# Kernel tuning notes

Hardware: AMD Instinct MI355X
Metric: run time of the kernel (lower is better)

Reference implementation:

```python
import jax, jax.numpy as jnp
import numpy as np

N_NODES, N_EDGES, N_ROOTS = 32768, 131072, 1024
VOCAB, EMB_D, FEAT = 50000, 256, 128
SEQ, HEADS, OUT_CH = 16, 16, 125
KERNELS = (5, 6, 7, 8)


def _add_self_loops(edge_index, n):
    loop = jnp.arange(n, dtype=edge_index.dtype)
    src = jnp.concatenate([edge_index[0], loop])
    dst = jnp.concatenate([edge_index[1], loop])
    return src, dst


def _gat_conv(x, W, a_src, a_dst, b, src, dst, n):
    # PyG GATConv (heads=1): h=xW, e_ij = LeakyReLU(a_s.h_j + a_d.h_i), softmax over incoming edges of i
    h = x @ W                                   # [N, F]
    al_s = h @ a_src                            # [N]
    al_d = h @ a_dst                            # [N]
    e = jax.nn.leaky_relu(al_s[src] + al_d[dst], 0.2)   # [E+N]
    m = jax.ops.segment_max(e, dst, num_segments=n)
    ex = jnp.exp(e - m[dst])
    den = jax.ops.segment_sum(ex, dst, num_segments=n)
    coef = ex / den[dst]
    out = jax.ops.segment_sum(coef[:, None] * h[src], dst, num_segments=n)
    return out + b


def _gcn_conv(x, W, b, src, dst, n):
    h = x @ W
    ones = jnp.ones_like(src, dtype=x.dtype)
    deg = jax.ops.segment_sum(ones, dst, num_segments=n)
    dinv = jax.lax.rsqrt(jnp.maximum(deg, 1.0))
    norm = dinv[src] * dinv[dst]                # [E+N]
    out = jax.ops.segment_sum(norm[:, None] * h[src], dst, num_segments=n)
    return out + b


def _transformer_block(x, Wq, bq, Wk, bk, Wv, bv, Wo, bo, g, be):
    # multi-head self-attention + output proj + residual + layernorm (attn_dropout=0)
    n, s, d = x.shape
    dh = d // HEADS
    q = (x @ Wq + bq).reshape(n, s, HEADS, dh)
    k = (x @ Wk + bk).reshape(n, s, HEADS, dh)
    v = (x @ Wv + bv).reshape(n, s, HEADS, dh)
    att = jnp.einsum('nqhd,nkhd->nhqk', q, k) / np.sqrt(dh).astype(np.float32)
    att = jax.nn.softmax(att, axis=-1)
    o = jnp.einsum('nhqk,nkhd->nqhd', att, v).reshape(n, s, d)
    o = o @ Wo + bo
    y = x + o
    mu = jnp.mean(y, axis=-1, keepdims=True)
    var = jnp.var(y, axis=-1, keepdims=True)
    return (y - mu) * jax.lax.rsqrt(var + 1e-5) * g + be


def _conv_branch(t, ws, bs):
    # t: [N, D, S]; Conv1d VALID + ReLU + max-pool over full output length
    feats = []
    for w, b in zip(ws, bs):
        a = jax.lax.conv_general_dilated(t, w, (1,), 'VALID',
                                         dimension_numbers=('NCH', 'OIH', 'NCH'))
        a = jax.nn.relu(a + b[:, None])
        feats.append(jnp.max(a, axis=-1))       # [N, OUT_CH]
    return jnp.concatenate(feats, axis=1)        # [N, 4*OUT_CH]


def _forward(x2, emb, Wq, bq, Wk, bk, Wv, bv, Wo, bo, ln_g, ln_b,
             gat1_W, gat1_as, gat1_ad, gat1_b, gcn1_W, gcn1_b,
             gat2_W, gat2_as, gat2_ad, gat2_b, gcn2_W, gcn2_b,
             conv_w0, conv_b0, conv_w1, conv_b1, conv_w2, conv_b2, conv_w3, conv_b3,
             fc1_W, fc1_b, fc2_W, fc2_b,
             text2, edge_index, root_index, rootpost_index):
    n = x2.shape[0]
    src, dst = _add_self_loops(edge_index, n)

    stance_graph = _gat_conv(x2, gat1_W, gat1_as, gat1_ad, gat1_b, src, dst, n)
    stance_shared = _gcn_conv(x2, gcn1_W, gcn1_b, src, dst, n)

    t = emb[text2]                                            # [N, S, D]
    t = _transformer_block(t, Wq, bq, Wk, bk, Wv, bv, Wo, bo, ln_g, ln_b)
    t_avg = jnp.mean(t, axis=1)                               # [N, D]

    cat = jnp.concatenate([stance_graph, stance_shared, t_avg], axis=1)  # [N, 2F+D]
    stance_graph2 = _gat_conv(cat, gat2_W, gat2_as, gat2_ad, gat2_b, src, dst, n)
    _ = _gcn_conv(stance_shared, gcn2_W, gcn2_b, src, dst, n)  # computed but unused in forward (faithful)

    tc = jnp.transpose(t, (0, 2, 1))                          # [N, D, S]
    text_feat = _conv_branch(tc, (conv_w0, conv_w1, conv_w2, conv_w3),
                             (conv_b0, conv_b1, conv_b2, conv_b3))  # [N, 500]

    final = jnp.concatenate([stance_graph2[root_index],
                             text_feat[root_index],
                             text_feat[rootpost_index]], axis=1)     # [B, F+1000]
    h = jax.nn.relu(final @ fc1_W + fc1_b)
    return h @ fc2_W + fc2_b                                  # [B, 3]


def setup_inputs() -> dict:
    key = jax.random.key(0)
    ks = iter(jax.random.split(key, 48))
    s = 0.05
    inp = {}
    inp['x2'] = jax.random.normal(next(ks), (N_NODES, FEAT), jnp.float32)
    inp['emb'] = jax.random.normal(next(ks), (VOCAB, EMB_D), jnp.float32) * s
    for nm in ['Wq', 'Wk', 'Wv', 'Wo']:
        inp[nm] = jax.random.normal(next(ks), (EMB_D, EMB_D), jnp.float32) * s
    for nm in ['bq', 'bk', 'bv', 'bo']:
        inp[nm] = jnp.zeros((EMB_D,), jnp.float32)
    inp['ln_g'] = jnp.ones((EMB_D,), jnp.float32)
    inp['ln_b'] = jnp.zeros((EMB_D,), jnp.float32)
    inp['gat1_W'] = jax.random.normal(next(ks), (FEAT, FEAT), jnp.float32) * s
    inp['gat1_as'] = jax.random.normal(next(ks), (FEAT,), jnp.float32) * s
    inp['gat1_ad'] = jax.random.normal(next(ks), (FEAT,), jnp.float32) * s
    inp['gat1_b'] = jnp.zeros((FEAT,), jnp.float32)
    inp['gcn1_W'] = jax.random.normal(next(ks), (FEAT, FEAT), jnp.float32) * s
    inp['gcn1_b'] = jnp.zeros((FEAT,), jnp.float32)
    inp['gat2_W'] = jax.random.normal(next(ks), (2 * FEAT + EMB_D, FEAT), jnp.float32) * s
    inp['gat2_as'] = jax.random.normal(next(ks), (FEAT,), jnp.float32) * s
    inp['gat2_ad'] = jax.random.normal(next(ks), (FEAT,), jnp.float32) * s
    inp['gat2_b'] = jnp.zeros((FEAT,), jnp.float32)
    inp['gcn2_W'] = jax.random.normal(next(ks), (FEAT, FEAT), jnp.float32) * s
    inp['gcn2_b'] = jnp.zeros((FEAT,), jnp.float32)
    for i, K in enumerate(KERNELS):
        inp[f'conv_w{i}'] = jax.random.normal(next(ks), (OUT_CH, EMB_D, K), jnp.float32) * s
        inp[f'conv_b{i}'] = jnp.zeros((OUT_CH,), jnp.float32)
    inp['fc1_W'] = jax.random.normal(next(ks), (FEAT + 8 * OUT_CH, 300), jnp.float32) * s
    inp['fc1_b'] = jnp.zeros((300,), jnp.float32)
    inp['fc2_W'] = jax.random.normal(next(ks), (300, 3), jnp.float32) * s
    inp['fc2_b'] = jnp.zeros((3,), jnp.float32)
    inp['text2'] = jax.random.randint(next(ks), (N_NODES, SEQ), 0, VOCAB, jnp.int32)
    inp['edge_index'] = jax.random.randint(next(ks), (2, N_EDGES), 0, N_NODES, jnp.int32)
    inp['root_index'] = jax.random.randint(next(ks), (N_ROOTS,), 0, N_NODES, jnp.int32)
    inp['rootpost_index'] = jax.random.randint(next(ks), (N_ROOTS,), 0, N_NODES, jnp.int32)
    return inp


def reference(x2, emb, Wq, bq, Wk, bk, Wv, bv, Wo, bo, ln_g, ln_b,
              gat1_W, gat1_as, gat1_ad, gat1_b, gcn1_W, gcn1_b,
              gat2_W, gat2_as, gat2_ad, gat2_b, gcn2_W, gcn2_b,
              conv_w0, conv_b0, conv_w1, conv_b1, conv_w2, conv_b2, conv_w3, conv_b3,
              fc1_W, fc1_b, fc2_W, fc2_b,
              text2, edge_index, root_index, rootpost_index):
    return _forward(x2, emb, Wq, bq, Wk, bk, Wv, bv, Wo, bo, ln_g, ln_b,
                    gat1_W, gat1_as, gat1_ad, gat1_b, gcn1_W, gcn1_b,
                    gat2_W, gat2_as, gat2_ad, gat2_b, gcn2_W, gcn2_b,
                    conv_w0, conv_b0, conv_w1, conv_b1, conv_w2, conv_b2, conv_w3, conv_b3,
                    fc1_W, fc1_b, fc2_W, fc2_b,
                    text2, edge_index, root_index, rootpost_index)
```

## Files before the change

### kernel.cpp

```cpp
#include <hip/hip_runtime.h>
#include <hip/hip_bf16.h>
#include <cstdint>
#include <cstddef>

#define N_NODES 32768
#define N_EDGES 131072
#define ET_EDGES (N_EDGES + N_NODES)
#define N_ROOTS 1024
#define EMB_D 256
#define FEAT 128
#define SEQ 16
#define OUT_CH 125

static inline int cdiv(long long a, long long b) { return (int)((a + b - 1) / b); }

typedef short short8 __attribute__((ext_vector_type(8)));
typedef short short4v __attribute__((ext_vector_type(4)));
typedef float f32x4 __attribute__((ext_vector_type(4)));

__device__ __forceinline__ float warpReduceSum(float v) {
#pragma unroll
    for (int m = 32; m; m >>= 1) v += __shfl_xor(v, m, 64);
    return v;
}
__device__ __forceinline__ int encf(float f) {
    int i = __float_as_int(f);
    return i >= 0 ? i : (i ^ 0x7fffffff);
}
__device__ __forceinline__ float decf(int i) {
    return __int_as_float(i >= 0 ? i : (i ^ 0x7fffffff));
}
__device__ __forceinline__ short f2bs(float x) {
    unsigned u = __float_as_uint(x);
    u += 0x7fffu + ((u >> 16) & 1u);
    return (short)(u >> 16);
}
__device__ __forceinline__ short2 f2bs2(float a, float b) {
    union {
        __hip_bfloat162 h;
        short2 s;
    } u;
    u.h = __float22bfloat162_rn(make_float2(a, b));
    return u.s;
}
__device__ __forceinline__ float bs2f(short s) {
    return __uint_as_float(((unsigned)(unsigned short)s) << 16);
}

__global__ void fill_i32(int* p, int v, int n) {
    int i = blockIdx.x * 256 + threadIdx.x;
    if (i < n) p[i] = v;
}

__global__ void init_cat(float* __restrict__ cat, const float* __restrict__ b1, const float* __restrict__ b2) {
    int i = blockIdx.x * 256 + threadIdx.x;
    int n = i >> 8, c = i & 255;
    float b = (c < 128) ? b1[c] : b2[c - 128];
    cat[(size_t)n * 512 + c] = b;
}

__global__ void repack_wall(const float* __restrict__ cw0, const float* __restrict__ cw1,
                            const float* __restrict__ cw2, const float* __restrict__ cw3,
                            __hip_bfloat16* __restrict__ wall) {
    int i = blockIdx.x * 256 + threadIdx.x;
    if (i >= 512 * 2048) return;
    int r = i >> 11, c = i & 2047;
    int k = c >> 8, ic = c & 255;
    float v = 0.f;
    if (r < 500) {
        int Kidx = r / 125, oc = r - Kidx * 125;
        int K = 5 + Kidx;
        if (k < K) {
            const float* cw = Kidx == 0 ? cw0 : Kidx == 1 ? cw1 : Kidx == 2 ? cw2 : cw3;
            v = cw[((size_t)oc * 256 + ic) * K + k];
        }
    }
    wall[i] = __float2bfloat16(v);
}

__global__ void repack_xf(const float* __restrict__ Wq, const float* __restrict__ Wk, const float* __restrict__ Wv,
                          const float* __restrict__ Wo, const float* __restrict__ bq, const float* __restrict__ bk,
                          const float* __restrict__ bv, short* __restrict__ wqkvT, short* __restrict__ woT,
                          float* __restrict__ bqkv) {
    int i = blockIdx.x * 256 + threadIdx.x;
    if (i < 768 * 256) {
        int n = i >> 8, k = i & 255;
        const float* W = n < 256 ? Wq : n < 512 ? Wk : Wv;
        wqkvT[i] = f2bs(W[k * 256 + (n & 255)]);
    }
    if (i < 256 * 256) {
        int n = i >> 8, k = i & 255;
        woT[i] = f2bs(Wo[k * 256 + n]);
    }
    if (i < 768) bqkv[i] = i < 256 ? bq[i] : i < 512 ? bk[i - 256] : bv[i - 512];
}

__global__ void repack_wT(const float* __restrict__ W, short* __restrict__ out, int K, int N) {
    int i = blockIdx.x * 256 + threadIdx.x;
    if (i >= K * N) return;
    int n = i / K, k = i - n * K;
    out[i] = f2bs(W[(size_t)k * N + n]);
}

__global__ __launch_bounds__(256) void mfma_gemm_n128(const float* __restrict__ A, const short* __restrict__ Wt,
                                                      float* __restrict__ C, int K) {
    __shared__ short As[128 * 40];
    __shared__ short Bs[128 * 40];
    const int m0 = blockIdx.x * 128;
    const int tid = threadIdx.x;
    const int lane = tid & 63;
    const int wave = tid >> 6;
    const int wm = (wave >> 1) * 64, wn = (wave & 1) * 64;
    const int quad = lane >> 4, l16 = lane & 15;

    const int r0 = tid >> 2, kc = (tid & 3) * 8;
    const int r1 = r0 + 64;

    f32x4 acc[4][4];
#pragma unroll
    for (int i = 0; i < 4; i++)
#pragma unroll
        for (int j = 0; j < 4; j++) acc[i][j] = (f32x4){0.f, 0.f, 0.f, 0.f};

    for (int k0 = 0; k0 < K; k0 += 32) {
#pragma unroll
        for (int rr = 0; rr < 2; rr++) {
            const int r = rr ? r1 : r0;
            const float* pa = A + (size_t)(m0 + r) * K + k0 + kc;
            float4 a0 = ((const float4*)pa)[0], a1 = ((const float4*)pa)[1];
            short2 c0 = f2bs2(a0.x, a0.y), c1 = f2bs2(a0.z, a0.w), c2 = f2bs2(a1.x, a1.y), c3 = f2bs2(a1.z, a1.w);
            *(short8*)(As + r * 40 + kc) = (short8){c0.x, c0.y, c1.x, c1.y, c2.x, c2.y, c3.x, c3.y};
        }
        *(short8*)(Bs + r0 * 40 + kc) = *(const short8*)(Wt + (size_t)r0 * K + k0 + kc);
        *(short8*)(Bs + r1 * 40 + kc) = *(const short8*)(Wt + (size_t)r1 * K + k0 + kc);
        __syncthreads();
        short8 af[4], bfr[4];
#pragma unroll
        for (int i = 0; i < 4; i++) af[i] = *(const short8*)(As + (wm + i * 16 + l16) * 40 + quad * 8);
#pragma unroll
        for (int j = 0; j < 4; j++) bfr[j] = *(const short8*)(Bs + (wn + j * 16 + l16) * 40 + quad * 8);
#pragma unroll
        for (int i = 0; i < 4; i++)
#pragma unroll
            for (int j = 0; j < 4; j++)
                acc[i][j] = __builtin_amdgcn_mfma_f32_16x16x32_bf16(af[i], bfr[j], acc[i][j], 0, 0, 0);
        __syncthreads();
    }
#pragma unroll
    for (int i = 0; i < 4; i++) {
#pragma unroll
        for (int j = 0; j < 4; j++) {
            const int col = wn + j * 16 + l16;
            const size_t base = (size_t)(m0 + wm + i * 16 + quad * 4) * 128 + col;
#pragma unroll
            for (int r = 0; r < 4; r++) C[base + (size_t)r * 128] = acc[i][j][r];
        }
    }
}

__global__ __launch_bounds__(256) void gemm64(const float* __restrict__ A, const float* __restrict__ B,
                                              const float* __restrict__ bias, float* __restrict__ C,
                                              int M, int N, int K, int lda, int ldc, int doRelu) {
    __shared__ float As[16][65];
    __shared__ float Bs[16][65];
    const int bm = blockIdx.y * 64, bn = blockIdx.x * 64;
    const int tid = threadIdx.x;
    const int tx = tid & 15, ty = tid >> 4;
    float acc[4][4] = {};
    for (int k0 = 0; k0 < K; k0 += 16) {
#pragma unroll
        for (int j = 0; j < 4; j++) {
            int i = tid + j * 256;
            int kk = i & 15, m = i >> 4;
            int gr = bm + m, gc = k0 + kk;
            As[kk][m] = (gr < M && gc < K) ? A[(size_t)gr * lda + gc] : 0.f;
        }
#pragma unroll
        for (int j = 0; j < 4; j++) {
            int i = tid + j * 256;
            int n = i & 63, kk = i >> 6;
            int gr = k0 + kk, gc = bn + n;
            Bs[kk][n] = (gr < K && gc < N) ? B[(size_t)gr * N + gc] : 0.f;
        }
        __syncthreads();
#pragma unroll
        for (int kk = 0; kk < 16; kk++) {
            float a[4], b[4];
#pragma unroll
            for (int i2 = 0; i2 < 4; i2++) a[i2] = As[kk][ty * 4 + i2];
#pragma unroll
            for (int j2 = 0; j2 < 4; j2++) b[j2] = Bs[kk][tx * 4 + j2];
#pragma unroll
            for (int i2 = 0; i2 < 4; i2++)
#pragma unroll
                for (int j2 = 0; j2 < 4; j2++) acc[i2][j2] = fmaf(a[i2], b[j2], acc[i2][j2]);
        }
        __syncthreads();
    }
#pragma unroll
    for (int i2 = 0; i2 < 4; i2++) {
        int r = bm + ty * 4 + i2;
        if (r >= M) continue;
#pragma unroll
        for (int j2 = 0; j2 < 4; j2++) {
            int c = bn + tx * 4 + j2;
            if (c >= N) continue;
            float v = acc[i2][j2];
            if (bias) v += bias[c];
            if (doRelu) v = fmaxf(v, 0.f);
            C[(size_t)r * ldc + c] = v;
        }
    }
}

__global__ __launch_bounds__(256) void alpha_kernel(const float* __restrict__ h, const float* __restrict__ asrc,
                                                    const float* __restrict__ adst, float* __restrict__ als,
                                                    float* __restrict__ ald) {
    int gw = (blockIdx.x * 256 + threadIdx.x) >> 6;
    int lane = threadIdx.x & 63;
    if (gw >= N_NODES) return;
    const float* row = h + (size_t)gw * FEAT;
    float v0 = row[lane], v1 = row[lane + 64];
    float ps = v0 * asrc[lane] + v1 * asrc[lane + 64];
    float pd = v0 * adst[lane] + v1 * adst[lane + 64];
    ps = warpReduceSum(ps);
    pd = warpReduceSum(pd);
    if (lane == 0) {
        als[gw] = ps;
        ald[gw] = pd;
    }
}

__device__ __forceinline__ void edge_decode(int i, const int* __restrict__ ei, int& s, int& d) {
    if (i < N_EDGES) {
        s = ei[i];
        d = ei[N_EDGES + i];
    } else {
        s = d = i - N_EDGES;
    }
}

__global__ void edge_p1(const int* __restrict__ ei, const float* __restrict__ als, const float* __restrict__ ald,
                        float* __restrict__ elog, int* __restrict__ menc, float* dega) {
    int i = blockIdx.x * 256 + threadIdx.x;
    if (i >= ET_EDGES) return;
    int s, d;
    edge_decode(i, ei, s, d);
    float e = als[s] + ald[d];
    e = (e >= 0.f) ? e : 0.2f * e;
    elog[i] = e;
    atomicMax(&menc[d], encf(e));
    if (dega) unsafeAtomicAdd(&dega[d], 1.f);
}

__global__ void edge_p2(const int* __restrict__ ei, float* __restrict__ elog, const int* __restrict__ menc,
                        float* __restrict__ den) {
    int i = blockIdx.x * 256 + threadIdx.x;
    if (i >= ET_EDGES) return;
    int s, d;
    edge_decode(i, ei, s, d);
    float ex = __expf(elog[i] - decf(menc[d]));
    elog[i] = ex;
    unsafeAtomicAdd(&den[d], ex);
}

__global__ void edge_p2b(const int* __restrict__ ei, float* __restrict__ elog, const float* __restrict__ den) {
    int i = blockIdx.x * 256 + threadIdx.x;
    if (i >= ET_EDGES) return;
    int s, d;
    edge_decode(i, ei, s, d);
    elog[i] = elog[i] / den[d];
}

__global__ void dinv_kernel(float* deg) {
    int i = blockIdx.x * 256 + threadIdx.x;
    if (i < N_NODES) deg[i] = rsqrtf(fmaxf(deg[i], 1.f));
}

__global__ void edge_scatter(const int* __restrict__ ei, const float* __restrict__ coef, const float* __restrict__ h,
                             float* __restrict__ out, int ldo) {
    int i = blockIdx.x * 256 + threadIdx.x;
    if (i >= ET_EDGES * FEAT) return;
    int e = i >> 7, f = i & 127;
    int s, d;
    edge_decode(e, ei, s, d);
    unsafeAtomicAdd(&out[(size_t)d * ldo + f], coef[e] * h[(size_t)s * FEAT + f]);
}

__global__ void gcn_scatter(const int* __restrict__ ei, const float* __restrict__ dinv, const float* __restrict__ h,
                            float* __restrict__ out, int ldo) {
    int i = blockIdx.x * 256 + threadIdx.x;
    if (i >= ET_EDGES * FEAT) return;
    int e = i >> 7, f = i & 127;
    int s, d;
    edge_decode(e, ei, s, d);
    float coef = dinv[s] * dinv[d];
    unsafeAtomicAdd(&out[(size_t)d * ldo + f], coef * h[(size_t)s * FEAT + f]);
}

__global__ void root_gather(const float* __restrict__ g2, const int* __restrict__ rooti, const float* __restrict__ gb,
                            float* __restrict__ fin) {
    int i = blockIdx.x * 256 + threadIdx.x;
    if (i >= N_ROOTS * FEAT) return;
    int r = i >> 7, c = i & 127;
    fin[(size_t)r * 1128 + c] = g2[(size_t)rooti[r] * FEAT + c] + gb[c];
}

__global__ void fc2_kernel(const float* __restrict__ fch, const float* __restrict__ W, const float* __restrict__ b,
                           float* __restrict__ out) {
    int i = blockIdx.x * 256 + threadIdx.x;
    if (i >= N_ROOTS * 3) return;
    int r = i / 3, c = i - r * 3;
    float acc = b[c];
    for (int k = 0; k < 300; k++) acc = fmaf(fch[(size_t)r * 300 + k], W[k * 3 + c], acc);
    out[i] = acc;
}

__device__ __forceinline__ int lsw(int row, int col) {
    return row * 256 + (col ^ ((row & 7) << 3));
}

__device__ __forceinline__ int vt_addr(int d, int key) {
    return d * 32 + (((key & 24) ^ (((d ^ (d >> 2)) & 3) << 3)) | (key & 7));
}

template <int MODE>
__global__ __launch_bounds__(256, 3) void xformer_kernel(
    const float* __restrict__ emb, const int* __restrict__ text2, const short* __restrict__ wqkvT,
    const float* __restrict__ bqkv, const short* __restrict__ woT, const float* __restrict__ bo,
    const float* __restrict__ lng, const float* __restrict__ lnb, const int* __restrict__ rooti,
    const int* __restrict__ rpi, float* __restrict__ cat, unsigned short* __restrict__ tbuf) {
    __shared__ short qa[32 * 256];
    __shared__ short kreg[32 * 256];
    __shared__ short vbuf[32 * 256];

    const int tid = threadIdx.x;
    const int wave = tid >> 6, lane = tid & 63;
    const int quad = lane >> 4, l16 = lane & 15;

    int gnode[2];
#pragma unroll
    for (int m = 0; m < 2; m++) {
        int slot = blockIdx.x * 2 + m;
        gnode[m] = (MODE == 0) ? slot : ((slot < N_ROOTS) ? rooti[slot] : rpi[slot - N_ROOTS]);
    }

    {
        const int row = tid >> 3, seg = tid & 7;
        const int m = row >> 4, r = row & 15;
        const int tok = text2[gnode[m] * SEQ + r];
        const float* ep = emb + (size_t)tok * 256 + seg * 32;
#pragma unroll
        for (int j = 0; j < 4; j++) {
            float4 ea = ((const float4*)(ep + j * 8))[0];
            float4 eb = ((const float4*)(ep + j * 8))[1];
            short2 w0 = f2bs2(ea.x, ea.y), w1 = f2bs2(ea.z, ea.w);
            short2 w2 = f2bs2(eb.x, eb.y), w3 = f2bs2(eb.z, eb.w);
            *(short8*)(kreg + lsw(row, seg * 32 + j * 8)) =
                (short8){w0.x, w0.y, w1.x, w1.y, w2.x, w2.y, w3.x, w3.y};
        }
    }
    __syncthreads();

    auto run_gemm_h = [&](const short* __restrict__ W, int wrow0, const short* __restrict__ Albase,
                          f32x4(&acc)[2][2]) {
        const short* wb = W + (size_t)(wrow0 + l16) * 256 + quad * 8;
        short8 B[2][8];
#pragma unroll
        for (int k0 = 0; k0 < 8; k0++) {
            B[0][k0] = *(const short8*)(wb + k0 * 32);
            B[1][k0] = *(const short8*)(wb + (size_t)16 * 256 + k0 * 32);
        }
#pragma unroll
        for (int i = 0; i < 2; i++) {
            acc[i][0] = (f32x4){0.f, 0.f, 0.f, 0.f};
            acc[i][1] = (f32x4){0.f, 0.f, 0.f, 0.f};
        }
#pragma unroll
        for (int k0 = 0; k0 < 8; k0++) {
            short8 A0 = *(const short8*)(Albase + lsw(l16, k0 * 32 + quad * 8));
            short8 A1 = *(const short8*)(Albase + lsw(16 + l16, k0 * 32 + quad * 8));
            acc[0][0] = __builtin_amdgcn_mfma_f32_16x16x32_bf16(A0, B[0][k0], acc[0][0], 0, 0, 0);
            acc[0][1] = __builtin_amdgcn_mfma_f32_16x16x32_bf16(A1, B[0][k0], acc[0][1], 0, 0, 0);
            acc[1][0] = __builtin_amdgcn_mfma_f32_16x16x32_bf16(A0, B[1][k0], acc[1][0], 0, 0, 0);
            acc[1][1] = __builtin_amdgcn_mfma_f32_16x16x32_bf16(A1, B[1][k0], acc[1][1], 0, 0, 0);
        }
    };

    auto kpriv = [&](int row, int c) { return wave * 2048 + row * 64 + (c ^ ((row & 7) << 3)); };

    f32x4 acc[2][2];

#pragma unroll 1
    for (int hh = 0; hh < 2; hh++) {
        run_gemm_h(wqkvT, (wave * 4 + hh * 2) * 16, kreg, acc);
#pragma unroll
        for (int ii = 0; ii < 2; ii++) {
            const int col = (wave * 4 + hh * 2 + ii) * 16 + l16;
            const float b = bqkv[col];
#pragma unroll
            for (int m = 0; m < 2; m++) {
                const int rbase = m * 16 + quad * 4;
                short2 p01 = f2bs2((acc[ii][m][0] + b) * 0.25f, (acc[ii][m][1] + b) * 0.25f);
                short2 p23 = f2bs2((acc[ii][m][2] + b) * 0.25f, (acc[ii][m][3] + b) * 0.25f);
                qa[lsw(rbase + 0, col)] = p01.x;
                qa[lsw(rbase + 1, col)] = p01.y;
                qa[lsw(rbase + 2, col)] = p23.x;
                qa[lsw(rbase + 3, col)] = p23.y;
            }
        }
    }
#pragma unroll 1
    for (int hh = 0; hh < 2; hh++) {
        run_gemm_h(wqkvT, (16 + wave * 4 + hh * 2) * 16, kreg, acc);
#pragma unroll
        for (int ii = 0; ii < 2; ii++) {
            const int i = hh * 2 + ii;
            const int c = i * 16 + l16;
            const float b = bqkv[(16 + wave * 4 + i) * 16 + l16];
#pragma unroll
            for (int m = 0; m < 2; m++) {
                const int rbase = m * 16 + quad * 4;
                short2 p01 = f2bs2(acc[ii][m][0] + b, acc[ii][m][1] + b);
                short2 p23 = f2bs2(acc[ii][m][2] + b, acc[ii][m][3] + b);
                vbuf[kpriv(rbase + 0, c)] = p01.x;
                vbuf[kpriv(rbase + 1, c)] = p01.y;
                vbuf[kpriv(rbase + 2, c)] = p23.x;
                vbuf[kpriv(rbase + 3, c)] = p23.y;
            }
        }
    }

#pragma unroll
    for (int p = 0; p < 2; p++) {
#pragma unroll
        for (int i = 0; i < 4; i++) {
            const int h = wave * 4 + i;
            const int arow = p * 16 + l16;
            const int q8 = (quad & 1) * 8;
            short8 Af = *(const short8*)(vbuf + kpriv(arow, i * 16 + q8));
            short8 Bf = *(const short8*)(qa + lsw(arow, h * 16 + q8));
            if (quad >= 2) {
                Af = (short8){0, 0, 0, 0, 0, 0, 0, 0};
                Bf = (short8){0, 0, 0, 0, 0, 0, 0, 0};
            }
            f32x4 S = __builtin_amdgcn_mfma_f32_16x16x32_bf16(Af, Bf, (f32x4){0.f, 0.f, 0.f, 0.f}, 0, 0, 0);
            float mx = fmaxf(fmaxf(S[0], S[1]), fmaxf(S[2], S[3]));
            mx = fmaxf(mx, __shfl_xor(mx, 16));
            mx = fmaxf(mx, __shfl_xor(mx, 32));
            float e0 = __expf(S[0] - mx), e1 = __expf(S[1] - mx);
            float e2 = __expf(S[2] - mx), e3 = __expf(S[3] - mx);
            float sm = (e0 + e1) + (e2 + e3);
            sm += __shfl_xor(sm, 16);
            sm += __shfl_xor(sm, 32);
            const float inv = 1.f / sm;
            short2 p01 = f2bs2(e0 * inv, e1 * inv), p23 = f2bs2(e2 * inv, e3 * inv);
            *(short4v*)(qa + lsw(arow, h * 16 + quad * 4)) = (short4v){p01.x, p01.y, p23.x, p23.y};
        }
    }

#pragma unroll 1
    for (int hh = 0; hh < 2; hh++) {
        run_gemm_h(wqkvT, (32 + wave * 4 + hh * 2) * 16, kreg, acc);
#pragma unroll
        for (int ii = 0; ii < 2; ii++) {
            const int i = hh * 2 + ii;
            const int d = (wave * 4 + i) * 16 + l16;
            const float b = bqkv[(32 + wave * 4 + i) * 16 + l16];
#pragma unroll
            for (int m = 0; m < 2; m++) {
                const int rbase = m * 16 + quad * 4;
                short2 p01 = f2bs2(acc[ii][m][0] + b, acc[ii][m][1] + b);
                short2 p23 = f2bs2(acc[ii][m][2] + b, acc[ii][m][3] + b);
                *(short4v*)(vbuf + vt_addr(d, rbase)) = (short4v){p01.x, p01.y, p23.x, p23.y};
            }
        }
    }

#pragma unroll
    for (int p = 0; p < 2; p++) {
#pragma unroll
        for (int i = 0; i < 4; i++) {
            const int h = wave * 4 + i;
            const int arow = p * 16 + l16;
            const int q8 = (quad & 1) * 8;
            short8 BP = *(const short8*)(qa + lsw(arow, h * 16 + q8));
            short8 Av = *(const short8*)(vbuf + vt_addr(h * 16 + l16, p * 16 + q8));
            if (quad >= 2) {
                BP = (short8){0, 0, 0, 0, 0, 0, 0, 0};
                Av = (short8){0, 0, 0, 0, 0, 0, 0, 0};
            }
            f32x4 O = __builtin_amdgcn_mfma_f32_16x16x32_bf16(Av, BP, (f32x4){0.f, 0.f, 0.f, 0.f}, 0, 0, 0);
            short2 o01 = f2bs2(O[0], O[1]), o23 = f2bs2(O[2], O[3]);
            *(short4v*)(qa + lsw(arow, h * 16 + quad * 4)) = (short4v){o01.x, o01.y, o23.x, o23.y};
        }
    }
    __syncthreads();

#pragma unroll 1
    for (int hh = 0; hh < 2; hh++) {
        run_gemm_h(woT, (wave * 4 + hh * 2) * 16, qa, acc);
#pragma unroll
        for (int ii = 0; ii < 2; ii++) {
            const int col = (wave * 4 + hh * 2 + ii) * 16 + l16;
            const float bocol = bo[col];
#pragma unroll
            for (int m = 0; m < 2; m++) {
                const int rbase = m * 16 + quad * 4;
                short2 a01 = f2bs2(acc[ii][m][0] + bocol, acc[ii][m][1] + bocol);
                short2 a23 = f2bs2(acc[ii][m][2] + bocol, acc[ii][m][3] + bocol);
                kreg[lsw(rbase + 0, col)] = a01.x;
                kreg[lsw(rbase + 1, col)] = a01.y;
                kreg[lsw(rbase + 2, col)] = a23.x;
                kreg[lsw(rbase + 3, col)] = a23.y;
            }
        }
    }
    __syncthreads();

    float* qs = (float*)qa;
    {
        const int row = tid >> 3, seg = tid & 7;
        const int m = row >> 4, r = row & 15;
        const int tokr = text2[gnode[m] * SEQ + r];
        const float* ep = emb + (size_t)tokr * 256 + seg * 32;
        float sum = 0.f, sq = 0.f;
#pragma unroll
        for (int j = 0; j < 4; j++) {
            const int base = lsw(row, seg * 32 + j * 8);
            short8 y8 = *(const short8*)(kreg + base);
            float4 ea = ((const float4*)(ep + j * 8))[0];
            float4 eb = ((const float4*)(ep + j * 8))[1];
            float evv[8] = {ea.x, ea.y, ea.z, ea.w, eb.x, eb.y, eb.z, eb.w};
            float yv[8];
#pragma unroll
            for (int e = 0; e < 8; e++) {
                yv[e] = bs2f(y8[e]) + evv[e];
                sum += yv[e];
                sq = fmaf(yv[e], yv[e], sq);
            }
            short2 w0 = f2bs2(yv[0], yv[1]), w1 = f2bs2(yv[2], yv[3]);
            short2 w2 = f2bs2(yv[4], yv[5]), w3 = f2bs2(yv[6], yv[7]);
            *(short4v*)(kreg + base) = (short4v){w0.x, w0.y, w1.x, w1.y};
            *(short4v*)(kreg + base + 4) = (short4v){w2.x, w2.y, w3.x, w3.y};
        }
        qs[tid] = sum;
        qs[256 + tid] = sq;
    }
    __syncthreads();
    if (tid < 32) {
        float s = 0.f, q2 = 0.f;
#pragma unroll
        for (int j = 0; j < 8; j++) {
            s += qs[tid * 8 + j];
            q2 += qs[256 + tid * 8 + j];
        }
        float mu = s * (1.f / 256.f);
        float var = q2 * (1.f / 256.f) - mu * mu;
        qs[512 + tid * 2] = mu;
        qs[512 + tid * 2 + 1] = rsqrtf(var + 1e-5f);
    }
    __syncthreads();
    {
        const int c = tid;
        const float g = lng[c], bb = lnb[c];
        float csum[2] = {0.f, 0.f};
#pragma unroll
        for (int m = 0; m < 2; m++) {
#pragma unroll
            for (int r = 0; r < 16; r++) {
                const int row = m * 16 + r;
                const float yv = bs2f(kreg[lsw(row, c)]);
                const float mu = qs[512 + row * 2], rstd = qs[512 + row * 2 + 1];
                const float o = (yv - mu) * rstd * g + bb;
                if (MODE == 0) {
                    csum[m] += o;
                } else {
                    tbuf[((size_t)(blockIdx.x * 2 + m) * 24 + r) * 256 + c] = (unsigned short)f2bs(o);
                }
            }
        }
        if (MODE == 0) {
            cat[(size_t)gnode[0] * 512 + 256 + c] = csum[0] * (1.f / 16.f);
            cat[(size_t)gnode[1] * 512 + 256 + c] = csum[1] * (1.f / 16.f);
        } else {
            for (int z = tid; z < 2 * 8 * 256; z += 256) {
                const int m = z >> 11, rem = z & 2047;
                tbuf[((size_t)(blockIdx.x * 2 + m) * 24 + 16 + (rem >> 8)) * 256 + (rem & 255)] = 0;
            }
        }
    }
}

__global__ __launch_bounds__(256) void conv_gemm(const short* __restrict__ tb, const short* __restrict__ wall,
                                                 float* __restrict__ C) {
    __shared__ short As[128 * 40];
    __shared__ short Bs[128 * 40];
    const int bid = blockIdx.x;
    const int m0 = (bid >> 2) * 128;
    const int n0 = (bid & 3) * 128;
    const int tid = threadIdx.x;
    const int lane = tid & 63;
    const int wave = tid >> 6;
    const int wm = (wave >> 1) * 64, wn = (wave & 1) * 64;
    const int quad = lane >> 4, l16 = lane & 15;

    const int r0 = tid >> 2, kc = (tid & 3) * 8;
    const int r1 = r0 + 64;
    const int am0 = m0 + r0, am1 = m0 + r1;
    const int s0 = am0 / 12, p0_ = am0 - s0 * 12;
    const int s1 = am1 / 12, p1_ = am1 - s1 * 12;
    const size_t ga0 = (size_t)(s0 * 24 + p0_) * 256 + kc;
    const size_t ga1 = (size_t)(s1 * 24 + p1_) * 256 + kc;
    const size_t gb0 = (size_t)(n0 + r0) * 2048 + kc;
    const size_t gb1 = (size_t)(n0 + r1) * 2048 + kc;
    short* sa0 = As + r0 * 40 + kc;
    short* sa1 = As + r1 * 40 + kc;
    short* sb0 = Bs + r0 * 40 + kc;
    short* sb1 = Bs + r1 * 40 + kc;

    f32x4 acc[4][4];
#pragma unroll
    for (int i = 0; i < 4; i++)
#pragma unroll
        for (int j = 0; j < 4; j++) acc[i][j] = (f32x4){0.f, 0.f, 0.f, 0.f};

    for (int k0 = 0; k0 < 2048; k0 += 32) {
        short8 a0 = *(const short8*)(tb + ga0 + k0);
        short8 a1 = *(const short8*)(tb + ga1 + k0);
        short8 b0 = *(const short8*)(wall + gb0 + k0);
        short8 b1 = *(const short8*)(wall + gb1 + k0);
        *(short8*)sa0 = a0;
        *(short8*)sa1 = a1;
        *(short8*)sb0 = b0;
        *(short8*)sb1 = b1;
        __syncthreads();
        short8 af[4], bfr[4];
#pragma unroll
        for (int i = 0; i < 4; i++) af[i] = *(const short8*)(As + (wm + i * 16 + l16) * 40 + quad * 8);
#pragma unroll
        for (int j = 0; j < 4; j++) bfr[j] = *(const short8*)(Bs + (wn + j * 16 + l16) * 40 + quad * 8);
#pragma unroll
        for (int i = 0; i < 4; i++)
#pragma unroll
            for (int j = 0; j < 4; j++)
                acc[i][j] = __builtin_amdgcn_mfma_f32_16x16x32_bf16(af[i], bfr[j], acc[i][j], 0, 0, 0);
        __syncthreads();
    }
#pragma unroll
    for (int i = 0; i < 4; i++) {
#pragma unroll
        for (int j = 0; j < 4; j++) {
            const int col = n0 + wn + j * 16 + l16;
            const size_t base = (size_t)(m0 + wm + i * 16 + quad * 4) * 512 + col;
#pragma unroll
            for (int r = 0; r < 4; r++) C[base + (size_t)r * 512] = acc[i][j][r];
        }
    }
}

__global__ void conv_maxpool(const float* __restrict__ C, const float* __restrict__ cb0, const float* __restrict__ cb1,
                             const float* __restrict__ cb2, const float* __restrict__ cb3, float* __restrict__ fin) {
    int i = blockIdx.x * 256 + threadIdx.x;
    if (i >= 2048 * 500) return;
    int slot = i / 500, q = i - slot * 500;
    int Kidx = q / 125, oc = q - Kidx * 125;
    int L = 12 - Kidx;
    const float* base = C + (size_t)(slot * 12) * 512 + q;
    float m = base[0];
    for (int p = 1; p < L; p++) m = fmaxf(m, base[(size_t)p * 512]);
    float b = (Kidx == 0 ? cb0 : Kidx == 1 ? cb1 : Kidx == 2 ? cb2 : cb3)[oc];
    float v = fmaxf(m + b, 0.f);
    int idx = slot < N_ROOTS ? slot : slot - N_ROOTS;
    int colbase = slot < N_ROOTS ? 128 : 628;
    fin[(size_t)idx * 1128 + colbase + q] = v;
}

extern "C" void kernel_launch(void* const* d_in, const int* in_sizes, int n_in, void* d_out, int out_size, void* d_ws,
                              size_t ws_size, hipStream_t stream) {
    const float* x2 = (const float*)d_in[0];
    const float* emb = (const float*)d_in[1];
    const float* Wq = (const float*)d_in[2];
    const float* Wk = (const float*)d_in[3];
    const float* Wv = (const float*)d_in[4];
    const float* Wo = (const float*)d_in[5];
    const float* bq = (const float*)d_in[6];
    const float* bk = (const float*)d_in[7];
    const float* bv = (const float*)d_in[8];
    const float* bo = (const float*)d_in[9];
    const float* lng = (const float*)d_in[10];
    const float* lnb = (const float*)d_in[11];
    const float* gat1_W = (const float*)d_in[12];
    const float* gat1_as = (const float*)d_in[13];
    const float* gat1_ad = (const float*)d_in[14];
    const float* gat1_b = (const float*)d_in[15];
    const float* gcn1_W = (const float*)d_in[16];
    const float* gcn1_b = (const float*)d_in[17];
    const float* gat2_W = (const float*)d_in[18];
    const float* gat2_as = (const float*)d_in[19];
    const float* gat2_ad = (const float*)d_in[20];
    const float* gat2_b = (const float*)d_in[21];
    const float* cw0 = (const float*)d_in[24];
    const float* cb0 = (const float*)d_in[25];
    const float* cw1 = (const float*)d_in[26];
    const float* cb1 = (const float*)d_in[27];
    const float* cw2 = (const float*)d_in[28];
    const float* cb2 = (const float*)d_in[29];
    const float* cw3 = (const float*)d_in[30];
    const float* cb3 = (const float*)d_in[31];
    const float* fc1_W = (const float*)d_in[32];
    const float* fc1_b = (const float*)d_in[33];
    const float* fc2_W = (const float*)d_in[34];
    const float* fc2_b = (const float*)d_in[35];
    const int* text2 = (const int*)d_in[36];
    const int* ei = (const int*)d_in[37];
    const int* rooti = (const int*)d_in[38];
    const int* rpi = (const int*)d_in[39];

    float* ws = (float*)d_ws;
    size_t off = 0;
    auto alloc = [&](size_t n) {
        float* p = ws + off;
        off += n;
        return p;
    };
    float* g2o = alloc((size_t)N_NODES * FEAT);
    float* den1 = alloc(N_NODES);
    float* den2 = alloc(N_NODES);
    float* deg = alloc(N_NODES);
    size_t zero_floats = off;
    float* cat = alloc((size_t)N_NODES * 512);
    float* h1 = alloc((size_t)N_NODES * FEAT);
    float* h2 = alloc((size_t)N_NODES * FEAT);
    float* hg2 = alloc((size_t)N_NODES * FEAT);
    float* als1 = alloc(N_NODES);
    float* ald1 = alloc(N_NODES);
    float* als2 = alloc(N_NODES);
    float* ald2 = alloc(N_NODES);
    int* m1 = (int*)alloc(N_NODES);
    int* m2 = (int*)alloc(N_NODES);
    float* el1 = alloc(ET_EDGES);
    float* el2 = alloc(ET_EDGES);
    float* fin = alloc((size_t)N_ROOTS * 1128);
    float* fch = alloc((size_t)N_ROOTS * 300);
    float* wallf = alloc(512 * 2048 / 2);
    float* wqkvTf = alloc(768 * 256 / 2);
    float* woTf = alloc(256 * 256 / 2);
    float* bqkv = alloc(768);
    float* wg1Tf = alloc(128 * 128 / 2);
    float* wc1Tf = alloc(128 * 128 / 2);
    float* wg2Tf = alloc(128 * 512 / 2);
    (void)ws_size;
    (void)in_sizes;
    (void)n_in;
    (void)out_size;

    unsigned short* tbuf = (unsigned short*)h1;
    __hip_bfloat16* wall = (__hip_bfloat16*)wallf;
    short* wqkvT = (short*)wqkvTf;
    short* woT = (short*)woTf;
    short* wg1T = (short*)wg1Tf;
    short* wc1T = (short*)wc1Tf;
    short* wg2T = (short*)wg2Tf;
    float* Cbuf = cat;

    hipMemsetAsync(g2o, 0, zero_floats * sizeof(float), stream);
    init_cat<<<cdiv((long long)N_NODES * 256, 256), 256, 0, stream>>>(cat, gat1_b, gcn1_b);
    fill_i32<<<cdiv(2 * N_NODES, 256), 256, 0, stream>>>(m1, (int)0x80000000, 2 * N_NODES);
    repack_wall<<<cdiv(512 * 2048, 256), 256, 0, stream>>>(cw0, cw1, cw2, cw3, wall);
    repack_xf<<<cdiv(768 * 256, 256), 256, 0, stream>>>(Wq, Wk, Wv, Wo, bq, bk, bv, wqkvT, woT, bqkv);
    repack_wT<<<cdiv(128 * 128, 256), 256, 0, stream>>>(gat1_W, wg1T, 128, 128);
    repack_wT<<<cdiv(128 * 128, 256), 256, 0, stream>>>(gcn1_W, wc1T, 128, 128);
    repack_wT<<<cdiv(512 * 128, 256), 256, 0, stream>>>(gat2_W, wg2T, 512, 128);

    mfma_gemm_n128<<<N_NODES / 128, 256, 0, stream>>>(x2, wg1T, h1, 128);
    mfma_gemm_n128<<<N_NODES / 128, 256, 0, stream>>>(x2, wc1T, h2, 128);
    alpha_kernel<<<cdiv((long long)N_NODES * 64, 256), 256, 0, stream>>>(h1, gat1_as, gat1_ad, als1, ald1);
    edge_p1<<<cdiv(ET_EDGES, 256), 256, 0, stream>>>(ei, als1, ald1, el1, m1, deg);
    edge_p2<<<cdiv(ET_EDGES, 256), 256, 0, stream>>>(ei, el1, m1, den1);
    edge_p2b<<<cdiv(ET_EDGES, 256), 256, 0, stream>>>(ei, el1, den1);
    dinv_kernel<<<cdiv(N_NODES, 256), 256, 0, stream>>>(deg);
    const int sc_blocks = cdiv((long long)ET_EDGES * FEAT, 256);
    edge_scatter<<<sc_blocks, 256, 0, stream>>>(ei, el1, h1, cat + 0, 512);
    gcn_scatter<<<sc_blocks, 256, 0, stream>>>(ei, deg, h2, cat + 128, 512);
    xformer_kernel<0><<<N_NODES / 2, 256, 0, stream>>>(emb, text2, wqkvT, bqkv, woT, bo, lng, lnb, rooti, rpi, cat,
                                                       nullptr);
    xformer_kernel<1><<<2 * N_ROOTS / 2, 256, 0, stream>>>(emb, text2, wqkvT, bqkv, woT, bo, lng, lnb, rooti, rpi,
                                                           nullptr, tbuf);
    mfma_gemm_n128<<<N_NODES / 128, 256, 0, stream>>>(cat, wg2T, hg2, 512);
    alpha_kernel<<<cdiv((long long)N_NODES * 64, 256), 256, 0, stream>>>(hg2, gat2_as, gat2_ad, als2, ald2);
    edge_p1<<<cdiv(ET_EDGES, 256), 256, 0, stream>>>(ei, als2, ald2, el2, m2, nullptr);
    edge_p2<<<cdiv(ET_EDGES, 256), 256, 0, stream>>>(ei, el2, m2, den2);
    edge_p2b<<<cdiv(ET_EDGES, 256), 256, 0, stream>>>(ei, el2, den2);
    edge_scatter<<<sc_blocks, 256, 0, stream>>>(ei, el2, hg2, g2o, FEAT);
    conv_gemm<<<192 * 4, 256, 0, stream>>>((const short*)tbuf, (const short*)wall, Cbuf);
    root_gather<<<cdiv(N_ROOTS * FEAT, 256), 256, 0, stream>>>(g2o, rooti, gat2_b, fin);
    conv_maxpool<<<cdiv(2048 * 500, 256), 256, 0, stream>>>(Cbuf, cb0, cb1, cb2, cb3, fin);
    gemm64<<<dim3(cdiv(300, 64), cdiv(N_ROOTS, 64)), 256, 0, stream>>>(fin, fc1_W, fc1_b, fch, N_ROOTS, 300, 1128,
                                                                       1128, 300, 1);
    fc2_kernel<<<cdiv(N_ROOTS * 3, 256), 256, 0, stream>>>(fch, fc2_W, fc2_b, (float*)d_out);
}
```

Measured before the change: 2.052 ms.

## Run transformer kernel with 512 threads, two heads per wave, streamed B loads

Doubles the transformer block size from 256 to 512 threads (8 waves), so each wave handles two heads instead of four. The GEMM helper now computes one 16-column tile per call and streams B fragments one k-step ahead instead of preloading all of them into registers. This cuts register pressure so more waves can be resident per CU, giving better latency hiding. LayerNorm and the reduction indexing are rewritten for 512 threads. In exchange each wave does less MFMA work between barriers, and B loads from global memory are exposed with only one step of prefetch.

```diff
diff --git a/kernel.cpp b/kernel.cpp
--- a/kernel.cpp
+++ b/kernel.cpp
@@ -325,7 +325,7 @@
 }
 
 template <int MODE>
-__global__ __launch_bounds__(256, 3) void xformer_kernel(
+__global__ __launch_bounds__(512, 6) void xformer_kernel(
     const float* __restrict__ emb, const int* __restrict__ text2, const short* __restrict__ wqkvT,
     const float* __restrict__ bqkv, const short* __restrict__ woT, const float* __restrict__ bo,
     const float* __restrict__ lng, const float* __restrict__ lnb, const int* __restrict__ rooti,
@@ -346,99 +346,87 @@
     }
 
     {
-        const int row = tid >> 3, seg = tid & 7;
+        const int row = tid >> 4, seg = tid & 15;
         const int m = row >> 4, r = row & 15;
         const int tok = text2[gnode[m] * SEQ + r];
-        const float* ep = emb + (size_t)tok * 256 + seg * 32;
-#pragma unroll
-        for (int j = 0; j < 4; j++) {
+        const float* ep = emb + (size_t)tok * 256 + seg * 16;
+#pragma unroll
+        for (int j = 0; j < 2; j++) {
             float4 ea = ((const float4*)(ep + j * 8))[0];
             float4 eb = ((const float4*)(ep + j * 8))[1];
             short2 w0 = f2bs2(ea.x, ea.y), w1 = f2bs2(ea.z, ea.w);
             short2 w2 = f2bs2(eb.x, eb.y), w3 = f2bs2(eb.z, eb.w);
-            *(short8*)(kreg + lsw(row, seg * 32 + j * 8)) =
+            *(short8*)(kreg + lsw(row, seg * 16 + j * 8)) =
                 (short8){w0.x, w0.y, w1.x, w1.y, w2.x, w2.y, w3.x, w3.y};
         }
     }
     __syncthreads();
 
-    auto run_gemm_h = [&](const short* __restrict__ W, int wrow0, const short* __restrict__ Albase,
-                          f32x4(&acc)[2][2]) {
+    auto run_gemm_1 = [&](const short* __restrict__ W, int wrow0, const short* __restrict__ Albase,
+                          f32x4(&acc)[2]) {
         const short* wb = W + (size_t)(wrow0 + l16) * 256 + quad * 8;
-        short8 B[2][8];
+        acc[0] = (f32x4){0.f, 0.f, 0.f, 0.f};
+        acc[1] = (f32x4){0.f, 0.f, 0.f, 0.f};
+        short8 Bc = *(const short8*)(wb);
 #pragma unroll
         for (int k0 = 0; k0 < 8; k0++) {
-            B[0][k0] = *(const short8*)(wb + k0 * 32);
-            B[1][k0] = *(const short8*)(wb + (size_t)16 * 256 + k0 * 32);
-        }
-#pragma unroll
-        for (int i = 0; i < 2; i++) {
-            acc[i][0] = (f32x4){0.f, 0.f, 0.f, 0.f};
-            acc[i][1] = (f32x4){0.f, 0.f, 0.f, 0.f};
-        }
-#pragma unroll
-        for (int k0 = 0; k0 < 8; k0++) {
+            short8 Bn;
+            if (k0 < 7) Bn = *(const short8*)(wb + (k0 + 1) * 32);
             short8 A0 = *(const short8*)(Albase + lsw(l16, k0 * 32 + quad * 8));
             short8 A1 = *(const short8*)(Albase + lsw(16 + l16, k0 * 32 + quad * 8));
-            acc[0][0] = __builtin_amdgcn_mfma_f32_16x16x32_bf16(A0, B[0][k0], acc[0][0], 0, 0, 0);
-            acc[0][1] = __builtin_amdgcn_mfma_f32_16x16x32_bf16(A1, B[0][k0], acc[0][1], 0, 0, 0);
-            acc[1][0] = __builtin_amdgcn_mfma_f32_16x16x32_bf16(A0, B[1][k0], acc[1][0], 0, 0, 0);
-            acc[1][1] = __builtin_amdgcn_mfma_f32_16x16x32_bf16(A1, B[1][k0], acc[1][1], 0, 0, 0);
+            acc[0] = __builtin_amdgcn_mfma_f32_16x16x32_bf16(A0, Bc, acc[0], 0, 0, 0);
+            acc[1] = __builtin_amdgcn_mfma_f32_16x16x32_bf16(A1, Bc, acc[1], 0, 0, 0);
+            Bc = Bn;
         }
     };
 
-    auto kpriv = [&](int row, int c) { return wave * 2048 + row * 64 + (c ^ ((row & 7) << 3)); };
-
-    f32x4 acc[2][2];
+    auto kpriv = [&](int row, int c) { return wave * 1024 + row * 32 + (c ^ ((row & 3) << 3)); };
+
+    f32x4 acc[2];
 
 #pragma unroll 1
-    for (int hh = 0; hh < 2; hh++) {
-        run_gemm_h(wqkvT, (wave * 4 + hh * 2) * 16, kreg, acc);
+    for (int ii = 0; ii < 2; ii++) {
+        const int h = wave * 2 + ii;
+        run_gemm_1(wqkvT, h * 16, kreg, acc);
+        const int col = h * 16 + l16;
+        const float b = bqkv[col];
+#pragma unroll
+        for (int m = 0; m < 2; m++) {
+            const int rbase = m * 16 + quad * 4;
+            short2 p01 = f2bs2((acc[m][0] + b) * 0.25f, (acc[m][1] + b) * 0.25f);
+            short2 p23 = f2bs2((acc[m][2] + b) * 0.25f, (acc[m][3] + b) * 0.25f);
+            qa[lsw(rbase + 0, col)] = p01.x;
+            qa[lsw(rbase + 1, col)] = p01.y;
+            qa[lsw(rbase + 2, col)] = p23.x;
+            qa[lsw(rbase + 3, col)] = p23.y;
+        }
+    }
+#pragma unroll 1
+    for (int ii = 0; ii < 2; ii++) {
+        const int h = wave * 2 + ii;
+        run_gemm_1(wqkvT, (16 + h) * 16, kreg, acc);
+        const int c = ii * 16 + l16;
+        const float b = bqkv[256 + h * 16 + l16];
+#pragma unroll
+        for (int m = 0; m < 2; m++) {
+            const int rbase = m * 16 + quad * 4;
+            short2 p01 = f2bs2(acc[m][0] + b, acc[m][1] + b);
+            short2 p23 = f2bs2(acc[m][2] + b, acc[m][3] + b);
+            vbuf[kpriv(rbase + 0, c)] = p01.x;
+            vbuf[kpriv(rbase + 1, c)] = p01.y;
+            vbuf[kpriv(rbase + 2, c)] = p23.x;
+            vbuf[kpriv(rbase + 3, c)] = p23.y;
+        }
+    }
+
+#pragma unroll
+    for (int p = 0; p < 2; p++) {
 #pragma unroll
         for (int ii = 0; ii < 2; ii++) {
-            const int col = (wave * 4 + hh * 2 + ii) * 16 + l16;
-            const float b = bqkv[col];
-#pragma unroll
-            for (int m = 0; m < 2; m++) {
-                const int rbase = m * 16 + quad * 4;
-                short2 p01 = f2bs2((acc[ii][m][0] + b) * 0.25f, (acc[ii][m][1] + b) * 0.25f);
-                short2 p23 = f2bs2((acc[ii][m][2] + b) * 0.25f, (acc[ii][m][3] + b) * 0.25f);
-                qa[lsw(rbase + 0, col)] = p01.x;
-                qa[lsw(rbase + 1, col)] = p01.y;
-                qa[lsw(rbase + 2, col)] = p23.x;
-                qa[lsw(rbase + 3, col)] = p23.y;
-            }
-        }
-    }
-#pragma unroll 1
-    for (int hh = 0; hh < 2; hh++) {
-        run_gemm_h(wqkvT, (16 + wave * 4 + hh * 2) * 16, kreg, acc);
-#pragma unroll
-        for (int ii = 0; ii < 2; ii++) {
-            const int i = hh * 2 + ii;
-            const int c = i * 16 + l16;
-            const float b = bqkv[(16 + wave * 4 + i) * 16 + l16];
-#pragma unroll
-            for (int m = 0; m < 2; m++) {
-                const int rbase = m * 16 + quad * 4;
-                short2 p01 = f2bs2(acc[ii][m][0] + b, acc[ii][m][1] + b);
-                short2 p23 = f2bs2(acc[ii][m][2] + b, acc[ii][m][3] + b);
-                vbuf[kpriv(rbase + 0, c)] = p01.x;
-                vbuf[kpriv(rbase + 1, c)] = p01.y;
-                vbuf[kpriv(rbase + 2, c)] = p23.x;
-                vbuf[kpriv(rbase + 3, c)] = p23.y;
-            }
-        }
-    }
-
-#pragma unroll
-    for (int p = 0; p < 2; p++) {
-#pragma unroll
-        for (int i = 0; i < 4; i++) {
-            const int h = wave * 4 + i;
+            const int h = wave * 2 + ii;
             const int arow = p * 16 + l16;
             const int q8 = (quad & 1) * 8;
-            short8 Af = *(const short8*)(vbuf + kpriv(arow, i * 16 + q8));
+            short8 Af = *(const short8*)(vbuf + kpriv(arow, ii * 16 + q8));
             short8 Bf = *(const short8*)(qa + lsw(arow, h * 16 + q8));
             if (quad >= 2) {
                 Af = (short8){0, 0, 0, 0, 0, 0, 0, 0};
@@ -460,28 +448,25 @@
     }
 
 #pragma unroll 1
-    for (int hh = 0; hh < 2; hh++) {
-        run_gemm_h(wqkvT, (32 + wave * 4 + hh * 2) * 16, kreg, acc);
+    for (int ii = 0; ii < 2; ii++) {
+        const int h = wave * 2 + ii;
+        run_gemm_1(wqkvT, (32 + h) * 16, kreg, acc);
+        const int d = h * 16 + l16;
+        const float b = bqkv[512 + h * 16 + l16];
+#pragma unroll
+        for (int m = 0; m < 2; m++) {
+            const int rbase = m * 16 + quad * 4;
+            short2 p01 = f2bs2(acc[m][0] + b, acc[m][1] + b);
+            short2 p23 = f2bs2(acc[m][2] + b, acc[m][3] + b);
+            *(short4v*)(vbuf + vt_addr(d, rbase)) = (short4v){p01.x, p01.y, p23.x, p23.y};
+        }
+    }
+
+#pragma unroll
+    for (int p = 0; p < 2; p++) {
 #pragma unroll
         for (int ii = 0; ii < 2; ii++) {
-            const int i = hh * 2 + ii;
-            const int d = (wave * 4 + i) * 16 + l16;
-            const float b = bqkv[(32 + wave * 4 + i) * 16 + l16];
-#pragma unroll
-            for (int m = 0; m < 2; m++) {
-                const int rbase = m * 16 + quad * 4;
-                short2 p01 = f2bs2(acc[ii][m][0] + b, acc[ii][m][1] + b);
-                short2 p23 = f2bs2(acc[ii][m][2] + b, acc[ii][m][3] + b);
-                *(short4v*)(vbuf + vt_addr(d, rbase)) = (short4v){p01.x, p01.y, p23.x, p23.y};
-            }
-        }
-    }
-
-#pragma unroll
-    for (int p = 0; p < 2; p++) {
-#pragma unroll
-        for (int i = 0; i < 4; i++) {
-            const int h = wave * 4 + i;
+            const int h = wave * 2 + ii;
             const int arow = p * 16 + l16;
             const int q8 = (quad & 1) * 8;
             short8 BP = *(const short8*)(qa + lsw(arow, h * 16 + q8));
@@ -498,36 +483,34 @@
     __syncthreads();
 
 #pragma unroll 1
-    for (int hh = 0; hh < 2; hh++) {
-        run_gemm_h(woT, (wave * 4 + hh * 2) * 16, qa, acc);
-#pragma unroll
-        for (int ii = 0; ii < 2; ii++) {
-            const int col = (wave * 4 + hh * 2 + ii) * 16 + l16;
-            const float bocol = bo[col];
-#pragma unroll
-            for (int m = 0; m < 2; m++) {
-                const int rbase = m * 16 + quad * 4;
-                short2 a01 = f2bs2(acc[ii][m][0] + bocol, acc[ii][m][1] + bocol);
-                short2 a23 = f2bs2(acc[ii][m][2] + bocol, acc[ii][m][3] + bocol);
-                kreg[lsw(rbase + 0, col)] = a01.x;
-                kreg[lsw(rbase + 1, col)] = a01.y;
-                kreg[lsw(rbase + 2, col)] = a23.x;
-                kreg[lsw(rbase + 3, col)] = a23.y;
-            }
+    for (int ii = 0; ii < 2; ii++) {
+        const int h = wave * 2 + ii;
+        run_gemm_1(woT, h * 16, qa, acc);
+        const int col = h * 16 + l16;
+        const float bocol = bo[col];
+#pragma unroll
+        for (int m = 0; m < 2; m++) {
+            const int rbase = m * 16 + quad * 4;
+            short2 a01 = f2bs2(acc[m][0] + bocol, acc[m][1] + bocol);
+            short2 a23 = f2bs2(acc[m][2] + bocol, acc[m][3] + bocol);
+            kreg[lsw(rbase + 0, col)] = a01.x;
+            kreg[lsw(rbase + 1, col)] = a01.y;
+            kreg[lsw(rbase + 2, col)] = a23.x;
+            kreg[lsw(rbase + 3, col)] = a23.y;
         }
     }
     __syncthreads();
 
     float* qs = (float*)qa;
     {
-        const int row = tid >> 3, seg = tid & 7;
+        const int row = tid >> 4, seg = tid & 15;
         const int m = row >> 4, r = row & 15;
         const int tokr = text2[gnode[m] * SEQ + r];
-        const float* ep = emb + (size_t)tokr * 256 + seg * 32;
+        const float* ep = emb + (size_t)tokr * 256 + seg * 16;
         float sum = 0.f, sq = 0.f;
 #pragma unroll
-        for (int j = 0; j < 4; j++) {
-            const int base = lsw(row, seg * 32 + j * 8);
+        for (int j = 0; j < 2; j++) {
+            const int base = lsw(row, seg * 16 + j * 8);
             short8 y8 = *(const short8*)(kreg + base);
             float4 ea = ((const float4*)(ep + j * 8))[0];
             float4 eb = ((const float4*)(ep + j * 8))[1];
@@ -545,48 +528,45 @@
             *(short4v*)(kreg + base + 4) = (short4v){w2.x, w2.y, w3.x, w3.y};
         }
         qs[tid] = sum;
-        qs[256 + tid] = sq;
+        qs[512 + tid] = sq;
     }
     __syncthreads();
     if (tid < 32) {
         float s = 0.f, q2 = 0.f;
 #pragma unroll
-        for (int j = 0; j < 8; j++) {
-            s += qs[tid * 8 + j];
-            q2 += qs[256 + tid * 8 + j];
+        for (int j = 0; j < 16; j++) {
+            s += qs[tid * 16 + j];
+            q2 += qs[512 + tid * 16 + j];
         }
         float mu = s * (1.f / 256.f);
         float var = q2 * (1.f / 256.f) - mu * mu;
-        qs[512 + tid * 2] = mu;
-        qs[512 + tid * 2 + 1] = rsqrtf(var + 1e-5f);
+        qs[1024 + tid * 2] = mu;
+        qs[1024 + tid * 2 + 1] = rsqrtf(var + 1e-5f);
     }
     __syncthreads();
     {
-        const int c = tid;
+        const int c = tid & 255;
+        const int m = tid >> 8;
         const float g = lng[c], bb = lnb[c];
-        float csum[2] = {0.f, 0.f};
-#pragma unroll
-        for (int m = 0; m < 2; m++) {
-#pragma unroll
-            for (int r = 0; r < 16; r++) {
-                const int row = m * 16 + r;
-                const float yv = bs2f(kreg[lsw(row, c)]);
-                const float mu = qs[512 + row * 2], rstd = qs[512 + row * 2 + 1];
-                const float o = (yv - mu) * rstd * g + bb;
-                if (MODE == 0) {
-                    csum[m] += o;
-                } else {
-                    tbuf[((size_t)(blockIdx.x * 2 + m) * 24 + r) * 256 + c] = (unsigned short)f2bs(o);
-                }
+        float csum = 0.f;
+#pragma unroll
+        for (int r = 0; r < 16; r++) {
+            const int row = m * 16 + r;
+            const float yv = bs2f(kreg[lsw(row, c)]);
+            const float mu = qs[1024 + row * 2], rstd = qs[1024 + row * 2 + 1];
+            const float o = (yv - mu) * rstd * g + bb;
+            if (MODE == 0) {
+                csum += o;
+            } else {
+                tbuf[((size_t)(blockIdx.x * 2 + m) * 24 + r) * 256 + c] = (unsigned short)f2bs(o);
             }
         }
         if (MODE == 0) {
-            cat[(size_t)gnode[0] * 512 + 256 + c] = csum[0] * (1.f / 16.f);
-            cat[(size_t)gnode[1] * 512 + 256 + c] = csum[1] * (1.f / 16.f);
+            cat[(size_t)gnode[m] * 512 + 256 + c] = csum * (1.f / 16.f);
         } else {
-            for (int z = tid; z < 2 * 8 * 256; z += 256) {
-                const int m = z >> 11, rem = z & 2047;
-                tbuf[((size_t)(blockIdx.x * 2 + m) * 24 + 16 + (rem >> 8)) * 256 + (rem & 255)] = 0;
+            for (int z = tid; z < 2 * 8 * 256; z += 512) {
+                const int mm = z >> 11, rem = z & 2047;
+                tbuf[((size_t)(blockIdx.x * 2 + mm) * 24 + 16 + (rem >> 8)) * 256 + (rem & 255)] = 0;
             }
         }
     }
@@ -783,9 +763,9 @@
     const int sc_blocks = cdiv((long long)ET_EDGES * FEAT, 256);
     edge_scatter<<<sc_blocks, 256, 0, stream>>>(ei, el1, h1, cat + 0, 512);
     gcn_scatter<<<sc_blocks, 256, 0, stream>>>(ei, deg, h2, cat + 128, 512);
-    xformer_kernel<0><<<N_NODES / 2, 256, 0, stream>>>(emb, text2, wqkvT, bqkv, woT, bo, lng, lnb, rooti, rpi, cat,
+    xformer_kernel<0><<<N_NODES / 2, 512, 0, stream>>>(emb, text2, wqkvT, bqkv, woT, bo, lng, lnb, rooti, rpi, cat,
                                                        nullptr);
-    xformer_kernel<1><<<2 * N_ROOTS / 2, 256, 0, stream>>>(emb, text2, wqkvT, bqkv, woT, bo, lng, lnb, rooti, rpi,
+    xformer_kernel<1><<<2 * N_ROOTS / 2, 512, 0, stream>>>(emb, text2, wqkvT, bqkv, woT, bo, lng, lnb, rooti, rpi,
                                                            nullptr, tbuf);
     mfma_gemm_n128<<<N_NODES / 128, 256, 0, stream>>>(cat, wg2T, hg2, 512);
     alpha_kernel<<<cdiv((long long)N_NODES * 64, 256), 256, 0, stream>>>(hg2, gat2_as, gat2_ad, als2, ald2);
```

Result: slower. 2.972 ms (+44.8%).
